# Kernel optimization log

Measured on AMD Instinct MI355X. Metric: run time of the kernel, lower is better.

## Reference

```python
import jax, jax.numpy as jnp
import numpy as np

K = 5  # top-k neighbors (init kwarg k)
EPS = 1e-12

def _normalize(x):
    n = jnp.linalg.norm(x, axis=1, keepdims=True)
    return x / jnp.maximum(n, EPS)

def setup_inputs() -> dict:
    key = jax.random.key(0)
    k1, k2, k3 = jax.random.split(key, 3)
    B, D, N, C = 1024, 1024, 100000, 1000
    features = jax.random.normal(k1, (B, D), dtype=jnp.float32)
    idx = jax.random.randint(k2, (B,), 0, N, dtype=jnp.int64)
    # buffers: feat_memory = F.normalize(rand(N, D)); pred_memory = ones(N, C)/C
    feat_memory = _normalize(jax.random.uniform(k3, (N, D), dtype=jnp.float32))
    pred_memory = jnp.ones((N, C), dtype=jnp.float32) / C
    return {"features": features, "idx": idx,
            "feat_memory": feat_memory, "pred_memory": pred_memory}

def reference(features, idx, feat_memory, pred_memory):
    B = features.shape[0]
    x = _normalize(features)                       # [B, D]
    dis = x @ feat_memory.T                        # [B, N] similarity
    # self-mask: each row's own bank entry set to global min (min is invariant
    # under this assignment, so the per-row torch loop vectorizes exactly)
    m = jnp.min(dis)
    dis = dis.at[jnp.arange(B), idx].set(m)
    _, indices = jax.lax.top_k(dis, K)             # [B, K]
    mean_logits = jnp.mean(pred_memory[indices], axis=1)  # [B, C]
    pseudo_labels = jnp.argmax(mean_logits, axis=1)       # [B]
    return pseudo_labels, mean_logits
```

## Files before the change

kernel.cpp:

```cpp
#include <hip/hip_runtime.h>
#include <stdint.h>
#include <stddef.h>

#define B_ROWS 1024
#define D_DIM  1024
#define N_MEM  100000
#define C_CLS  1000
#define K_TOP  5

#define TM 128
#define TN 128
#define BK 32
#define NT_TILES ((N_MEM + TN - 1) / TN)
#define BT_TILES (B_ROWS / TM)
#define NPAD (NT_TILES * TN)
#define NTL_PER_XCD ((NT_TILES + 7) / 8)
#define SS_LD (TN + 4)

typedef __bf16 bf16;
typedef bf16 bf16x4 __attribute__((ext_vector_type(4)));
typedef bf16 bf16x8 __attribute__((ext_vector_type(8)));
typedef float f32x4 __attribute__((ext_vector_type(4)));

__device__ __forceinline__ void insert5(float v, int n, float tv[K_TOP], int ti[K_TOP]) {
#pragma unroll
  for (int j = 0; j < K_TOP; ++j) {
    bool gt = v > tv[j];
    float ov = tv[j]; int oi = ti[j];
    tv[j] = gt ? v : ov;  ti[j] = gt ? n : oi;
    v = gt ? ov : v;      n = gt ? oi : n;
  }
}

__global__ __launch_bounds__(256) void k_normalize(const float* __restrict__ F,
                                                   bf16* __restrict__ X) {
  int row = blockIdx.x;
  int tid = threadIdx.x;
  const float4* fr = (const float4*)(F + (size_t)row * D_DIM);
  float4 v = fr[tid];
  float s = v.x * v.x + v.y * v.y + v.z * v.z + v.w * v.w;
  for (int off = 32; off > 0; off >>= 1) s += __shfl_down(s, off, 64);
  __shared__ float wred[4];
  if ((tid & 63) == 0) wred[tid >> 6] = s;
  __syncthreads();
  float tot = wred[0] + wred[1] + wred[2] + wred[3];
  float inv = 1.0f / fmaxf(sqrtf(tot), 1e-12f);
  bf16x4 o;
  o[0] = (bf16)(v.x * inv);
  o[1] = (bf16)(v.y * inv);
  o[2] = (bf16)(v.z * inv);
  o[3] = (bf16)(v.w * inv);
  *(bf16x4*)(X + (size_t)row * D_DIM + (size_t)tid * 4) = o;
}

__global__ __launch_bounds__(256) void k_convert(const float* __restrict__ FM,
                                                 bf16* __restrict__ FMB, int total4) {
  int i = blockIdx.x * 256 + threadIdx.x;
  if (i >= total4) return;
  float4 v = ((const float4*)FM)[i];
  bf16x4 o;
  o[0] = (bf16)v.x; o[1] = (bf16)v.y; o[2] = (bf16)v.z; o[3] = (bf16)v.w;
  ((bf16x4*)FMB)[i] = o;
}

__device__ __forceinline__ void gl_lds16(const bf16* g, bf16* l) {
  __builtin_amdgcn_global_load_lds((__attribute__((address_space(1))) void*)g,
                                   (__attribute__((address_space(3))) void*)l,
                                   16, 0, 0);
}

__global__ __launch_bounds__(256) void k_gemm_topk(const bf16* __restrict__ X,
                                                   const bf16* __restrict__ FMB,
                                                   const int* __restrict__ IDX,
                                                   float2* __restrict__ CAND) {
  __shared__ __align__(16) char shm[2 * TM * BK * 2];
  __shared__ bf16 Ss[TM * SS_LD];
  bf16* As = (bf16*)shm;
  bf16* Bs = As + TM * BK;

  int bid = blockIdx.x;
  int xcd = bid & 7;
  int rest = bid >> 3;
  int bt = rest & 7;
  int ntl = rest >> 3;
  int nt = xcd * NTL_PER_XCD + ntl;
  if (nt >= NT_TILES) return;

  size_t row0 = (size_t)bt * TM;
  size_t col0 = (size_t)nt * TN;
  int tid = threadIdx.x;
  int lane = tid & 63;
  int wv = tid >> 6;
  int wm = wv >> 1, wn = wv & 1;

  f32x4 acc[4][4];
  for (int mi = 0; mi < 4; ++mi)
    for (int ni = 0; ni < 4; ++ni)
      acc[mi][ni] = (f32x4){0.f, 0.f, 0.f, 0.f};

  int frow = lane & 15;
  int q = lane >> 4;

  const bf16* Xbase = X + row0 * D_DIM;
  const bf16* Fbase = FMB + col0 * D_DIM;

  for (int k0 = 0; k0 < D_DIM; k0 += BK) {
    __syncthreads();
    for (int r = 0; r < 2; ++r) {
      int c = r * 256 + tid;
      int arow = c >> 2;
      int j = (c & 3) ^ ((arow >> 1) & 3);
      gl_lds16(Xbase + (size_t)arow * D_DIM + k0 + j * 8, As + (size_t)c * 8);
      gl_lds16(Fbase + (size_t)arow * D_DIM + k0 + j * 8, Bs + (size_t)c * 8);
    }
    __syncthreads();

    bf16x8 af[4], bfr[4];
    for (int mi = 0; mi < 4; ++mi) {
      int r = wm * 64 + mi * 16 + frow;
      int slot = r * 4 + (q ^ ((r >> 1) & 3));
      af[mi] = *(const bf16x8*)&As[(size_t)slot * 8];
    }
    for (int ni = 0; ni < 4; ++ni) {
      int r = wn * 64 + ni * 16 + frow;
      int slot = r * 4 + (q ^ ((r >> 1) & 3));
      bfr[ni] = *(const bf16x8*)&Bs[(size_t)slot * 8];
    }
    for (int mi = 0; mi < 4; ++mi)
      for (int ni = 0; ni < 4; ++ni)
        acc[mi][ni] = __builtin_amdgcn_mfma_f32_16x16x32_bf16(af[mi], bfr[ni],
                                                              acc[mi][ni], 0, 0, 0);
  }

  int orow = (lane >> 4) * 4;
  int ocol = lane & 15;
  for (int mi = 0; mi < 4; ++mi)
    for (int ni = 0; ni < 4; ++ni)
      for (int r = 0; r < 4; ++r)
        Ss[(size_t)(wm * 64 + mi * 16 + orow + r) * SS_LD + (wn * 64 + ni * 16 + ocol)]
            = (bf16)acc[mi][ni][r];
  __syncthreads();

  int tr = tid >> 1, h = tid & 1;
  int grow = (int)row0 + tr;
  int self = IDX[grow];
  float tv[K_TOP]; int ti[K_TOP];
  for (int j = 0; j < K_TOP; ++j) { tv[j] = -1e30f; ti[j] = -1; }
  for (int c = 0; c < 64; ++c) {
    int cc = h * 64 + c;
    int gc = (int)col0 + cc;
    if (gc >= N_MEM || gc == self) continue;
    float v = (float)Ss[(size_t)tr * SS_LD + cc];
    if (v > tv[K_TOP - 1]) insert5(v, gc, tv, ti);
  }

  float* mv = (float*)shm;
  int* mi_ = (int*)(shm + 8192);
  for (int j = 0; j < K_TOP; ++j) { mv[tid * K_TOP + j] = tv[j]; mi_[tid * K_TOP + j] = ti[j]; }
  __syncthreads();
  if (h == 0) {
    for (int j = 0; j < K_TOP; ++j) {
      float v = mv[(tid + 1) * K_TOP + j];
      int n = mi_[(tid + 1) * K_TOP + j];
      if (v > tv[K_TOP - 1]) insert5(v, n, tv, ti);
    }
    float2* out = CAND + ((size_t)grow * NT_TILES + nt) * K_TOP;
    for (int j = 0; j < K_TOP; ++j)
      out[j] = make_float2(tv[j], __int_as_float(ti[j]));
  }
}

__device__ void gather_mean_argmax(const int* find, const float* __restrict__ P,
                                   float* __restrict__ OUT, int b, int tid) {
  float bestV = -1e30f;
  int bestC = 0;
  for (int c = tid; c < C_CLS; c += 256) {
    float s = 0.f;
    for (int j = 0; j < K_TOP; ++j) s += P[(size_t)find[j] * C_CLS + c];
    float mean = s * (1.0f / K_TOP);
    OUT[(size_t)B_ROWS + (size_t)b * C_CLS + c] = mean;
    if (mean > bestV) { bestV = mean; bestC = c; }
  }
  __shared__ float rv[256];
  __shared__ int rc[256];
  rv[tid] = bestV; rc[tid] = bestC;
  for (int s = 128; s >= 1; s >>= 1) {
    __syncthreads();
    if (tid < s) {
      float v2 = rv[tid + s]; int c2 = rc[tid + s];
      if (v2 > rv[tid] || (v2 == rv[tid] && c2 < rc[tid])) { rv[tid] = v2; rc[tid] = c2; }
    }
  }
  __syncthreads();
  if (tid == 0) OUT[b] = (float)rc[0];
}

__global__ __launch_bounds__(256) void k_merge(const float2* __restrict__ CAND,
                                               const float* __restrict__ P,
                                               float* __restrict__ OUT) {
  int b = blockIdx.x;
  int tid = threadIdx.x;
  const float2* row = CAND + (size_t)b * (NT_TILES * K_TOP);

  float tv[K_TOP]; int ti[K_TOP];
  for (int j = 0; j < K_TOP; ++j) { tv[j] = -1e30f; ti[j] = -1; }
  for (int i = tid; i < NT_TILES * K_TOP; i += 256) {
    float2 e = row[i];
    float v = e.x;
    if (v > tv[K_TOP - 1]) insert5(v, __float_as_int(e.y), tv, ti);
  }

  __shared__ float sv[256 * K_TOP];
  __shared__ int si[256 * K_TOP];
  for (int j = 0; j < K_TOP; ++j) { sv[tid * K_TOP + j] = tv[j]; si[tid * K_TOP + j] = ti[j]; }
  for (int s = 128; s >= 1; s >>= 1) {
    __syncthreads();
    if (tid < s) {
      for (int j = 0; j < K_TOP; ++j) {
        float v = sv[(tid + s) * K_TOP + j];
        int n = si[(tid + s) * K_TOP + j];
        if (v > tv[K_TOP - 1]) insert5(v, n, tv, ti);
      }
      for (int j = 0; j < K_TOP; ++j) { sv[tid * K_TOP + j] = tv[j]; si[tid * K_TOP + j] = ti[j]; }
    }
  }
  __syncthreads();
  __shared__ int find[K_TOP];
  if (tid == 0)
    for (int j = 0; j < K_TOP; ++j) {
      int v = si[j];
      find[j] = (v < 0) ? 0 : (v >= N_MEM ? N_MEM - 1 : v);
    }
  __syncthreads();
  gather_mean_argmax(find, P, OUT, b, tid);
}

__global__ __launch_bounds__(256) void k_naive(const float* __restrict__ F,
                                               const int* __restrict__ IDX,
                                               const float* __restrict__ FM,
                                               const float* __restrict__ P,
                                               float* __restrict__ OUT) {
  int b = blockIdx.x;
  int tid = threadIdx.x;
  __shared__ float wred[4];
  const float4* fr = (const float4*)(F + (size_t)b * D_DIM);
  float4 v = fr[tid];
  float s = v.x * v.x + v.y * v.y + v.z * v.z + v.w * v.w;
  for (int off = 32; off > 0; off >>= 1) s += __shfl_down(s, off, 64);
  if ((tid & 63) == 0) wred[tid >> 6] = s;
  __syncthreads();
  float inv = 1.0f / fmaxf(sqrtf(wred[0] + wred[1] + wred[2] + wred[3]), 1e-12f);
  float4 xv = make_float4(v.x * inv, v.y * inv, v.z * inv, v.w * inv);
  __syncthreads();
  int self = IDX[b];
  __shared__ float ptv[K_TOP];
  __shared__ int pti[K_TOP];
  if (tid < K_TOP) { ptv[tid] = -1e30f; pti[tid] = 0; }
  __syncthreads();
  for (int n = 0; n < N_MEM; ++n) {
    const float4* frow = (const float4*)(FM + (size_t)n * D_DIM);
    float4 fv = frow[tid];
    float p = xv.x * fv.x + xv.y * fv.y + xv.z * fv.z + xv.w * fv.w;
    for (int off = 32; off > 0; off >>= 1) p += __shfl_down(p, off, 64);
    if ((tid & 63) == 0) wred[tid >> 6] = p;
    __syncthreads();
    if (tid == 0 && n != self) {
      float tot = wred[0] + wred[1] + wred[2] + wred[3];
      if (tot > ptv[K_TOP - 1]) {
        int q = K_TOP - 1;
        while (q > 0 && tot > ptv[q - 1]) { ptv[q] = ptv[q - 1]; pti[q] = pti[q - 1]; --q; }
        ptv[q] = tot; pti[q] = n;
      }
    }
    __syncthreads();
  }
  __shared__ int find[K_TOP];
  if (tid < K_TOP) {
    int x = pti[tid];
    find[tid] = (x < 0) ? 0 : (x >= N_MEM ? N_MEM - 1 : x);
  }
  __syncthreads();
  gather_mean_argmax(find, P, OUT, b, tid);
}

extern "C" void kernel_launch(void* const* d_in, const int* in_sizes, int n_in,
                              void* d_out, int out_size, void* d_ws, size_t ws_size,
                              hipStream_t stream) {
  const float* F  = (const float*)d_in[0];
  const int* IDX  = (const int*)d_in[1];
  const float* FM = (const float*)d_in[2];
  const float* P  = (const float*)d_in[3];
  float* OUT = (float*)d_out;

  const size_t xBytes    = (size_t)B_ROWS * D_DIM * 2;
  const size_t fmBytes   = (size_t)NPAD * D_DIM * 2;
  const size_t candBytes = (size_t)B_ROWS * NT_TILES * K_TOP * 8;
  const size_t need = xBytes + fmBytes + candBytes;

  if (ws_size >= need) {
    bf16* X      = (bf16*)d_ws;
    bf16* FMB    = (bf16*)((char*)d_ws + xBytes);
    float2* CAND = (float2*)((char*)d_ws + xBytes + fmBytes);
    k_normalize<<<B_ROWS, 256, 0, stream>>>(F, X);
    int total4 = N_MEM * D_DIM / 4;
    k_convert<<<(total4 + 255) / 256, 256, 0, stream>>>(FM, FMB, total4);
    k_gemm_topk<<<8 * NTL_PER_XCD * BT_TILES, 256, 0, stream>>>(X, FMB, IDX, CAND);
    k_merge<<<B_ROWS, 256, 0, stream>>>(CAND, P, OUT);
  } else {
    k_naive<<<B_ROWS, 256, 0, stream>>>(F, IDX, FM, P, OUT);
  }
}
```

Measured before the change: 1.076 ms.

## Use 256x256 double-buffered GEMM tiles with interleaved async staging and shuffle merge

Rebuilds the similarity GEMM as 256x256x64 block tiles run by 512 threads, using 128 KB of dynamic LDS as two buffers. The next k-tile's global-to-LDS loads are interleaved with MFMA phases, with manual vmcnt waits, barriers and s_setprio, to hide memory latency and raise operand reuse. The epilogue writes scores to a swizzled LDS layout and merges the two half-row top-5 lists with lane shuffles instead of a shared-memory round trip. The convert kernel now processes 8 elements per thread and zero-pads the bank to the tile size. The large LDS footprint limits occupancy to one block per CU, and the hand-written wait counts are fragile.

```diff
diff --git a/kernel.cpp b/kernel.cpp
--- a/kernel.cpp
+++ b/kernel.cpp
@@ -8,19 +8,26 @@
 #define C_CLS  1000
 #define K_TOP  5
 
-#define TM 128
-#define TN 128
-#define BK 32
-#define NT_TILES ((N_MEM + TN - 1) / TN)
-#define BT_TILES (B_ROWS / TM)
-#define NPAD (NT_TILES * TN)
-#define NTL_PER_XCD ((NT_TILES + 7) / 8)
-#define SS_LD (TN + 4)
+#define BM 256
+#define BN 256
+#define BKT 64
+#define NKT (D_DIM / BKT)
+#define NT_TILES ((N_MEM + BN - 1) / BN)
+#define NPAD (NT_TILES * BN)
+#define BT_TILES (B_ROWS / BM)
+#define NT_PER_XCD 49
+#define GRID_GEMM (8 * NT_PER_XCD * BT_TILES)
 
 typedef __bf16 bf16;
 typedef bf16 bf16x4 __attribute__((ext_vector_type(4)));
 typedef bf16 bf16x8 __attribute__((ext_vector_type(8)));
 typedef float f32x4 __attribute__((ext_vector_type(4)));
+
+#define MFMA16(a, b, c) __builtin_amdgcn_mfma_f32_16x16x32_bf16((a), (b), (c), 0, 0, 0)
+#define BARRIER() do { asm volatile("" ::: "memory"); \
+                       __builtin_amdgcn_s_barrier();  \
+                       asm volatile("" ::: "memory"); } while (0)
+#define WAITVM(N) asm volatile("s_waitcnt vmcnt(" #N ")" ::: "memory")
 
 __device__ __forceinline__ void insert5(float v, int n, float tv[K_TOP], int ti[K_TOP]) {
 #pragma unroll
@@ -54,117 +61,219 @@
 }
 
 __global__ __launch_bounds__(256) void k_convert(const float* __restrict__ FM,
-                                                 bf16* __restrict__ FMB, int total4) {
+                                                 bf16* __restrict__ FMB,
+                                                 int total8, int pad8) {
   int i = blockIdx.x * 256 + threadIdx.x;
-  if (i >= total4) return;
-  float4 v = ((const float4*)FM)[i];
-  bf16x4 o;
-  o[0] = (bf16)v.x; o[1] = (bf16)v.y; o[2] = (bf16)v.z; o[3] = (bf16)v.w;
-  ((bf16x4*)FMB)[i] = o;
-}
-
-__device__ __forceinline__ void gl_lds16(const bf16* g, bf16* l) {
+  if (i >= pad8) return;
+  bf16x8 o;
+  if (i < total8) {
+    float4 a = ((const float4*)FM)[2 * i];
+    float4 b = ((const float4*)FM)[2 * i + 1];
+    o[0] = (bf16)a.x; o[1] = (bf16)a.y; o[2] = (bf16)a.z; o[3] = (bf16)a.w;
+    o[4] = (bf16)b.x; o[5] = (bf16)b.y; o[6] = (bf16)b.z; o[7] = (bf16)b.w;
+  } else {
+#pragma unroll
+    for (int e = 0; e < 8; ++e) o[e] = (bf16)0.f;
+  }
+  ((bf16x8*)FMB)[i] = o;
+}
+
+__device__ __forceinline__ void gl_lds16(const bf16* g, char* l) {
   __builtin_amdgcn_global_load_lds((__attribute__((address_space(1))) void*)g,
                                    (__attribute__((address_space(3))) void*)l,
                                    16, 0, 0);
 }
 
-__global__ __launch_bounds__(256) void k_gemm_topk(const bf16* __restrict__ X,
-                                                   const bf16* __restrict__ FMB,
-                                                   const int* __restrict__ IDX,
-                                                   float2* __restrict__ CAND) {
-  __shared__ __align__(16) char shm[2 * TM * BK * 2];
-  __shared__ bf16 Ss[TM * SS_LD];
-  bf16* As = (bf16*)shm;
-  bf16* Bs = As + TM * BK;
-
+#define STAGE_HALF(g, off, rbase, k0) do {                                     \
+    gl_lds16((g) + (size_t)(rbase) * D_DIM + (k0),      lds + (off) + d0);     \
+    gl_lds16((g) + (size_t)((rbase) + 64) * D_DIM + (k0), lds + (off) + d1);   \
+  } while (0)
+
+__global__ __launch_bounds__(512, 2) void k_gemm_topk(const bf16* __restrict__ X,
+                                                      const bf16* __restrict__ FMB,
+                                                      const int* __restrict__ IDX,
+                                                      float2* __restrict__ CAND) {
+  extern __shared__ char lds[];
   int bid = blockIdx.x;
   int xcd = bid & 7;
-  int rest = bid >> 3;
-  int bt = rest & 7;
-  int ntl = rest >> 3;
-  int nt = xcd * NTL_PER_XCD + ntl;
-  if (nt >= NT_TILES) return;
-
-  size_t row0 = (size_t)bt * TM;
-  size_t col0 = (size_t)nt * TN;
+  int jj = bid >> 3;
+  int cnt = (xcd < 7) ? NT_PER_XCD : (NT_TILES - 7 * NT_PER_XCD);
+  if (jj >= 4 * cnt) return;
+  int nt = xcd * NT_PER_XCD + (jj >> 2);
+  int bt = jj & 3;
+  size_t row0 = (size_t)bt * BM;
+  size_t col0 = (size_t)nt * BN;
+
   int tid = threadIdx.x;
   int lane = tid & 63;
   int wv = tid >> 6;
-  int wm = wv >> 1, wn = wv & 1;
-
-  f32x4 acc[4][4];
-  for (int mi = 0; mi < 4; ++mi)
+  int wm = wv >> 2, wn = wv & 3;
+  int frow = lane & 15, q = lane >> 4;
+  int cs0 = ((q ^ (frow & 7)) * 16);
+  int cs1 = (((q + 4) ^ (frow & 7)) * 16);
+
+  int arow0 = tid >> 3;
+  int jsrc = (tid & 7) ^ (arow0 & 7);
+  const bf16* gA = X   + ((size_t)row0 + arow0) * D_DIM + jsrc * 8;
+  const bf16* gB = FMB + ((size_t)col0 + arow0) * D_DIM + jsrc * 8;
+  int d0 = tid * 16;
+  int d1 = 8192 + tid * 16;
+
+  STAGE_HALF(gA, 0,     0,   0);
+  STAGE_HALF(gA, 16384, 128, 0);
+  STAGE_HALF(gB, 32768, 0,   0);
+  STAGE_HALF(gB, 49152, 128, 0);
+  STAGE_HALF(gA, 65536 + 0,     0,   BKT);
+  STAGE_HALF(gA, 65536 + 16384, 128, BKT);
+  STAGE_HALF(gB, 65536 + 32768, 0,   BKT);
+  STAGE_HALF(gB, 65536 + 49152, 128, BKT);
+
+  f32x4 acc[8][4];
+#pragma unroll
+  for (int mi = 0; mi < 8; ++mi)
+#pragma unroll
     for (int ni = 0; ni < 4; ++ni)
       acc[mi][ni] = (f32x4){0.f, 0.f, 0.f, 0.f};
 
-  int frow = lane & 15;
-  int q = lane >> 4;
-
-  const bf16* Xbase = X + row0 * D_DIM;
-  const bf16* Fbase = FMB + col0 * D_DIM;
-
-  for (int k0 = 0; k0 < D_DIM; k0 += BK) {
-    __syncthreads();
-    for (int r = 0; r < 2; ++r) {
-      int c = r * 256 + tid;
-      int arow = c >> 2;
-      int j = (c & 3) ^ ((arow >> 1) & 3);
-      gl_lds16(Xbase + (size_t)arow * D_DIM + k0 + j * 8, As + (size_t)c * 8);
-      gl_lds16(Fbase + (size_t)arow * D_DIM + k0 + j * 8, Bs + (size_t)c * 8);
-    }
-    __syncthreads();
-
-    bf16x8 af[4], bfr[4];
+  WAITVM(8);
+  BARRIER();
+
+#pragma unroll 2
+  for (int kt = 0; kt < NKT; ++kt) {
+    char* buf = lds + ((kt & 1) << 16);
+    const char* Ab = buf + wm * 16384 + frow * 128;
+    const char* Bb = buf + 32768 + ((wn >> 1) * 16384) + ((wn & 1) * 8192) + frow * 128;
+    int bufoff = (kt & 1) << 16;
+    int k2 = (kt + 2) * BKT;
+    bool do_stage = (kt < NKT - 2);
+    bf16x8 af[4][2], bfr[4][2];
+
+#pragma unroll
     for (int mi = 0; mi < 4; ++mi) {
-      int r = wm * 64 + mi * 16 + frow;
-      int slot = r * 4 + (q ^ ((r >> 1) & 3));
-      af[mi] = *(const bf16x8*)&As[(size_t)slot * 8];
-    }
+      af[mi][0] = *(const bf16x8*)(Ab + mi * 2048 + cs0);
+      af[mi][1] = *(const bf16x8*)(Ab + mi * 2048 + cs1);
+    }
+#pragma unroll
+    for (int nb = 0; nb < 2; ++nb) {
+      bfr[nb][0] = *(const bf16x8*)(Bb + nb * 2048 + cs0);
+      bfr[nb][1] = *(const bf16x8*)(Bb + nb * 2048 + cs1);
+    }
+    BARRIER();
+    __builtin_amdgcn_s_setprio(1);
+#pragma unroll
+    for (int mi = 0; mi < 4; ++mi)
+#pragma unroll
+      for (int nb = 0; nb < 2; ++nb) {
+        acc[mi][nb] = MFMA16(af[mi][0], bfr[nb][0], acc[mi][nb]);
+        acc[mi][nb] = MFMA16(af[mi][1], bfr[nb][1], acc[mi][nb]);
+      }
+    __builtin_amdgcn_s_setprio(0);
+    BARRIER();
+
+#pragma unroll
+    for (int nb = 2; nb < 4; ++nb) {
+      bfr[nb][0] = *(const bf16x8*)(Bb + nb * 2048 + cs0);
+      bfr[nb][1] = *(const bf16x8*)(Bb + nb * 2048 + cs1);
+    }
+    BARRIER();
+    __builtin_amdgcn_s_setprio(1);
+#pragma unroll
+    for (int mi = 0; mi < 4; ++mi)
+#pragma unroll
+      for (int nb = 2; nb < 4; ++nb) {
+        acc[mi][nb] = MFMA16(af[mi][0], bfr[nb][0], acc[mi][nb]);
+        acc[mi][nb] = MFMA16(af[mi][1], bfr[nb][1], acc[mi][nb]);
+      }
+    __builtin_amdgcn_s_setprio(0);
+    BARRIER();
+
+#pragma unroll
+    for (int mi = 0; mi < 4; ++mi) {
+      af[mi][0] = *(const bf16x8*)(Ab + 8192 + mi * 2048 + cs0);
+      af[mi][1] = *(const bf16x8*)(Ab + 8192 + mi * 2048 + cs1);
+    }
+    if (do_stage) {
+      STAGE_HALF(gB, bufoff + 32768, 0,   k2);
+      STAGE_HALF(gB, bufoff + 49152, 128, k2);
+    }
+    BARRIER();
+    __builtin_amdgcn_s_setprio(1);
+#pragma unroll
+    for (int mi = 0; mi < 4; ++mi)
+#pragma unroll
+      for (int nb = 2; nb < 4; ++nb) {
+        acc[4 + mi][nb] = MFMA16(af[mi][0], bfr[nb][0], acc[4 + mi][nb]);
+        acc[4 + mi][nb] = MFMA16(af[mi][1], bfr[nb][1], acc[4 + mi][nb]);
+      }
+    __builtin_amdgcn_s_setprio(0);
+    BARRIER();
+
+    if (do_stage) {
+      STAGE_HALF(gA, bufoff + 0,     0,   k2);
+      STAGE_HALF(gA, bufoff + 16384, 128, k2);
+    }
+    BARRIER();
+    __builtin_amdgcn_s_setprio(1);
+#pragma unroll
+    for (int mi = 0; mi < 4; ++mi)
+#pragma unroll
+      for (int nb = 0; nb < 2; ++nb) {
+        acc[4 + mi][nb] = MFMA16(af[mi][0], bfr[nb][0], acc[4 + mi][nb]);
+        acc[4 + mi][nb] = MFMA16(af[mi][1], bfr[nb][1], acc[4 + mi][nb]);
+      }
+    __builtin_amdgcn_s_setprio(0);
+    if (kt < NKT - 2) { WAITVM(8); } else { WAITVM(0); }
+    BARRIER();
+  }
+
+  int Rbase = wm * 128 + q * 4;
+#pragma unroll
+  for (int mi = 0; mi < 8; ++mi)
+#pragma unroll
     for (int ni = 0; ni < 4; ++ni) {
-      int r = wn * 64 + ni * 16 + frow;
-      int slot = r * 4 + (q ^ ((r >> 1) & 3));
-      bfr[ni] = *(const bf16x8*)&Bs[(size_t)slot * 8];
-    }
-    for (int mi = 0; mi < 4; ++mi)
-      for (int ni = 0; ni < 4; ++ni)
-        acc[mi][ni] = __builtin_amdgcn_mfma_f32_16x16x32_bf16(af[mi], bfr[ni],
-                                                              acc[mi][ni], 0, 0, 0);
-  }
-
-  int orow = (lane >> 4) * 4;
-  int ocol = lane & 15;
-  for (int mi = 0; mi < 4; ++mi)
-    for (int ni = 0; ni < 4; ++ni)
-      for (int r = 0; r < 4; ++r)
-        Ss[(size_t)(wm * 64 + mi * 16 + orow + r) * SS_LD + (wn * 64 + ni * 16 + ocol)]
-            = (bf16)acc[mi][ni][r];
+      int Cc = wn * 64 + ni * 16 + frow;
+      int chunkC = Cc >> 3;
+      int e2 = (Cc & 7) * 2;
+#pragma unroll
+      for (int r = 0; r < 4; ++r) {
+        int R = Rbase + mi * 16 + r;
+        *(bf16*)(lds + R * 512 + ((chunkC ^ (R & 31)) * 16) + e2) = (bf16)acc[mi][ni][r];
+      }
+    }
   __syncthreads();
 
   int tr = tid >> 1, h = tid & 1;
   int grow = (int)row0 + tr;
   int self = IDX[grow];
   float tv[K_TOP]; int ti[K_TOP];
+#pragma unroll
   for (int j = 0; j < K_TOP; ++j) { tv[j] = -1e30f; ti[j] = -1; }
-  for (int c = 0; c < 64; ++c) {
-    int cc = h * 64 + c;
-    int gc = (int)col0 + cc;
-    if (gc >= N_MEM || gc == self) continue;
-    float v = (float)Ss[(size_t)tr * SS_LD + cc];
-    if (v > tv[K_TOP - 1]) insert5(v, gc, tv, ti);
-  }
-
-  float* mv = (float*)shm;
-  int* mi_ = (int*)(shm + 8192);
-  for (int j = 0; j < K_TOP; ++j) { mv[tid * K_TOP + j] = tv[j]; mi_[tid * K_TOP + j] = ti[j]; }
-  __syncthreads();
+  int swz = tr & 31;
+#pragma unroll
+  for (int c8 = 0; c8 < 16; ++c8) {
+    int chunk = h * 16 + c8;
+    bf16x8 v8 = *(const bf16x8*)(lds + tr * 512 + ((chunk ^ swz) * 16));
+#pragma unroll
+    for (int e = 0; e < 8; ++e) {
+      int gc = (int)col0 + chunk * 8 + e;
+      if (gc >= N_MEM || gc == self) continue;
+      float v = (float)v8[e];
+      if (v > tv[K_TOP - 1]) insert5(v, gc, tv, ti);
+    }
+  }
+  float pv[K_TOP]; int pi[K_TOP];
+#pragma unroll
+  for (int j = 0; j < K_TOP; ++j) {
+    pv[j] = __shfl_xor(tv[j], 1, 64);
+    pi[j] = __shfl_xor(ti[j], 1, 64);
+  }
+#pragma unroll
+  for (int j = 0; j < K_TOP; ++j)
+    if (pv[j] > tv[K_TOP - 1]) insert5(pv[j], pi[j], tv, ti);
+
   if (h == 0) {
-    for (int j = 0; j < K_TOP; ++j) {
-      float v = mv[(tid + 1) * K_TOP + j];
-      int n = mi_[(tid + 1) * K_TOP + j];
-      if (v > tv[K_TOP - 1]) insert5(v, n, tv, ti);
-    }
     float2* out = CAND + ((size_t)grow * NT_TILES + nt) * K_TOP;
+#pragma unroll
     for (int j = 0; j < K_TOP; ++j)
       out[j] = make_float2(tv[j], __int_as_float(ti[j]));
   }
@@ -298,13 +407,16 @@
   const size_t need = xBytes + fmBytes + candBytes;
 
   if (ws_size >= need) {
-    bf16* X      = (bf16*)d_ws;
+    bf16* Xb     = (bf16*)d_ws;
     bf16* FMB    = (bf16*)((char*)d_ws + xBytes);
     float2* CAND = (float2*)((char*)d_ws + xBytes + fmBytes);
-    k_normalize<<<B_ROWS, 256, 0, stream>>>(F, X);
-    int total4 = N_MEM * D_DIM / 4;
-    k_convert<<<(total4 + 255) / 256, 256, 0, stream>>>(FM, FMB, total4);
-    k_gemm_topk<<<8 * NTL_PER_XCD * BT_TILES, 256, 0, stream>>>(X, FMB, IDX, CAND);
+    (void)hipFuncSetAttribute((const void*)k_gemm_topk,
+                              hipFuncAttributeMaxDynamicSharedMemorySize, 131072);
+    k_normalize<<<B_ROWS, 256, 0, stream>>>(F, Xb);
+    int total8 = N_MEM * D_DIM / 8;
+    int pad8   = NPAD * D_DIM / 8;
+    k_convert<<<(pad8 + 255) / 256, 256, 0, stream>>>(FM, FMB, total8, pad8);
+    k_gemm_topk<<<GRID_GEMM, 512, 131072, stream>>>(Xb, FMB, IDX, CAND);
     k_merge<<<B_ROWS, 256, 0, stream>>>(CAND, P, OUT);
   } else {
     k_naive<<<B_ROWS, 256, 0, stream>>>(F, IDX, FM, P, OUT);
```

Measured after the change: 1.071 ms. Within noise of the previous version (-0.4%).
